# Kernel tuning notes

Hardware: AMD Instinct MI355X
Metric: run time of the kernel (lower is better)

Reference implementation:

```python
import jax, jax.numpy as jnp
import numpy as np

DIM = 1024   # dim
T = 16       # maximum_time_steps
NT = 64      # num_templates
B = 2048     # batch
S = 77       # words per sentence


def setup_inputs() -> dict:
    key = jax.random.key(0)
    ks = jax.random.split(key, 16)
    p = lambda k, shp: jax.random.normal(k, shp, dtype=jnp.float32) * 0.02
    return {
        "text_feats": jax.random.normal(ks[0], (B, S, DIM), dtype=jnp.float32),
        "text_sentence_feats": jax.random.normal(ks[1], (B, DIM), dtype=jnp.float32),
        "textual_query": jax.random.normal(ks[2], (B, DIM), dtype=jnp.float32),
        "time_step": jax.random.randint(ks[3], (B,), 0, T),
        "W1_w": p(ks[4], (T, DIM, DIM)),   # T stacked [out,in] linears
        "W1_b": p(ks[5], (T, DIM)),
        "W2_w": p(ks[6], (DIM, 2 * DIM)),
        "W2_b": p(ks[7], (DIM,)),
        "m1_w": p(ks[8], (DIM, DIM)),
        "m1_b": p(ks[9], (DIM,)),
        "m2_w": p(ks[10], (DIM, DIM)),
        "m2_b": p(ks[11], (DIM,)),
        "m3_w": p(ks[12], (NT, DIM)),
        "m3_b": p(ks[13], (NT,)),
        "attn_w": p(ks[14], (1, DIM)),
        "attn_b": p(ks[15], (1,)),
    }


def reference(text_feats, text_sentence_feats, textual_query, time_step,
              W1_w, W1_b, W2_w, W2_b, m1_w, m1_b, m2_w, m2_b, m3_w, m3_b,
              attn_w, attn_b):
    # Time-indexed linear: T is small, so compute all T projections for every
    # sample and select per-sample (avoids materializing a [B,DIM,DIM] gather).
    all_proj = jnp.einsum('bc,toc->tbo', text_sentence_feats, W1_w) + W1_b[:, None, :]  # t b d
    x1 = jnp.take_along_axis(all_proj, time_step[None, :, None], axis=0)[0]  # b d
    # concat with textual query, project back to dim
    x = jnp.concatenate([x1, textual_query], axis=-1) @ W2_w.T + W2_b  # b d
    # 3-layer MLP -> template distribution
    h = jax.nn.relu(x @ m1_w.T + m1_b)
    h = jax.nn.relu(h @ m2_w.T + m2_b)
    template_distribution = jax.nn.softmax(h @ m3_w.T + m3_b, axis=-1)  # b #templates
    # soft attention over words: score each (x * word_feat) with a linear
    x_w = x[:, None, :] * text_feats  # b s c
    scores = jnp.einsum('bsc,c->bs', x_w, attn_w[0]) + attn_b[0]
    words_soft_distribution = jax.nn.softmax(scores, axis=-1)  # b s
    c_t = jnp.einsum('bs,bsc->bc', words_soft_distribution, text_feats)  # b c
    return template_distribution, words_soft_distribution, c_t
```

## Files before the change

kernel.cpp:

```cpp
#include <hip/hip_runtime.h>
#include <stdint.h>

typedef __bf16 bf16;
typedef bf16 bf16x8 __attribute__((ext_vector_type(8)));
typedef bf16 bf16x4 __attribute__((ext_vector_type(4)));
typedef float f32x4 __attribute__((ext_vector_type(4)));

#define DIM   1024
#define TMAX  16
#define NTPL  64
#define BATCH 2048
#define SLEN  77

__device__ __forceinline__ void gl_lds16(const void* g, void* l) {
  __builtin_amdgcn_global_load_lds(
      (const __attribute__((address_space(1))) void*)g,
      (__attribute__((address_space(3))) void*)l, 16, 0, 0);
}

__global__ void bucket_k(const int* __restrict__ ts, int* __restrict__ perm,
                         int* __restrict__ bstart) {
  __shared__ int cnt[TMAX], base[TMAX], cur[TMAX];
  int tid = threadIdx.x;
  if (tid < TMAX) { cnt[tid] = 0; cur[tid] = 0; }
  __syncthreads();
  for (int b = tid; b < BATCH; b += 256) atomicAdd(&cnt[ts[b]], 1);
  __syncthreads();
  if (tid == 0) {
    int a = 0;
    for (int t = 0; t < TMAX; ++t) { base[t] = a; bstart[t] = a; a += cnt[t]; }
    bstart[TMAX] = a;
  }
  __syncthreads();
  for (int b = tid; b < BATCH; b += 256) {
    int t = ts[b];
    perm[base[t] + atomicAdd(&cur[t], 1)] = b;
  }
}

__global__ void cvt_bf16_k(const float* __restrict__ src, bf16* __restrict__ dst) {
  int idx = blockIdx.x * 256 + threadIdx.x;
  float4 v = ((const float4*)src)[idx];
  bf16x4 o = {(bf16)v.x, (bf16)v.y, (bf16)v.z, (bf16)v.w};
  ((bf16x4*)dst)[idx] = o;
}

__global__ void cvt_tq_k(const float* __restrict__ tq, bf16* __restrict__ xcat) {
  int idx = blockIdx.x * 256 + threadIdx.x;
  int b = idx >> 8, c4 = idx & 255;
  float4 v = ((const float4*)(tq + (size_t)b * DIM))[c4];
  bf16x4 o = {(bf16)v.x, (bf16)v.y, (bf16)v.z, (bf16)v.w};
  *(bf16x4*)(xcat + (size_t)b * 2 * DIM + DIM + c4 * 4) = o;
}

__global__ __launch_bounds__(256, 2) void gemm_bt(
    const bf16* __restrict__ A, int lda, const bf16* __restrict__ B, int ldb,
    const float* __restrict__ bias, bf16* __restrict__ C, int ldc,
    float* __restrict__ Cf, int N, int K, int relu) {
  __shared__ bf16 As[128 * 32];
  __shared__ bf16 Bs[128 * 32];
  const int tid = threadIdx.x;
  const int rowBase = blockIdx.y * 128, colBase = blockIdx.x * 128;

  const bf16* ag[2]; const bf16* bg[2];
  bf16* al[2]; bf16* bl[2];
#pragma unroll
  for (int i = 0; i < 2; ++i) {
    int j = tid + i * 256;
    int r = j >> 2, kq = j & 3;
    ag[i] = A + (size_t)(rowBase + r) * lda + kq * 8;
    int bn = colBase + r; if (bn > N - 1) bn = N - 1;
    bg[i] = B + (size_t)bn * ldb + kq * 8;
    al[i] = As + j * 8;
    bl[i] = Bs + j * 8;
  }
  const int wave = tid >> 6, lane = tid & 63;
  const int wm = wave >> 1, wn = wave & 1;
  const int mr = lane & 15, quad = lane >> 4;

  f32x4 acc[4][4];
#pragma unroll
  for (int i = 0; i < 4; ++i)
#pragma unroll
    for (int j = 0; j < 4; ++j) acc[i][j] = (f32x4){0.f, 0.f, 0.f, 0.f};

  for (int k0 = 0; k0 < K; k0 += 32) {
    __syncthreads();
#pragma unroll
    for (int i = 0; i < 2; ++i) {
      gl_lds16(ag[i] + k0, al[i]);
      gl_lds16(bg[i] + k0, bl[i]);
    }
    __syncthreads();
    bf16x8 af[4], bfr[4];
#pragma unroll
    for (int i = 0; i < 4; ++i)
      af[i] = *(const bf16x8*)&As[(wm * 64 + i * 16 + mr) * 32 + quad * 8];
#pragma unroll
    for (int j = 0; j < 4; ++j)
      bfr[j] = *(const bf16x8*)&Bs[(wn * 64 + j * 16 + mr) * 32 + quad * 8];
#pragma unroll
    for (int i = 0; i < 4; ++i)
#pragma unroll
      for (int j = 0; j < 4; ++j)
        acc[i][j] = __builtin_amdgcn_mfma_f32_16x16x32_bf16(af[i], bfr[j], acc[i][j], 0, 0, 0);
  }

  const int r0 = quad * 4;
#pragma unroll
  for (int i = 0; i < 4; ++i) {
    int gm = rowBase + wm * 64 + i * 16 + r0;
#pragma unroll
    for (int j = 0; j < 4; ++j) {
      int gn = colBase + wn * 64 + j * 16 + mr;
      if (gn < N) {
        float bv = bias ? bias[gn] : 0.f;
#pragma unroll
        for (int r = 0; r < 4; ++r) {
          float v = acc[i][j][r] + bv;
          if (relu) v = fmaxf(v, 0.f);
          C[(size_t)(gm + r) * ldc + gn] = (bf16)v;
          if (Cf) Cf[(size_t)(gm + r) * ldc + gn] = v;
        }
      }
    }
  }
}

__global__ __launch_bounds__(256, 2) void gemm_stage1(
    const bf16* __restrict__ tsbf, const bf16* __restrict__ W1bf,
    const float* __restrict__ W1b, const int* __restrict__ perm,
    const int* __restrict__ bstart, bf16* __restrict__ xcat) {
  const int t = blockIdx.z;
  const int s0 = bstart[t];
  const int cnt = bstart[t + 1] - s0;
  const int by = blockIdx.y;
  if (by * 128 >= cnt) return;
  __shared__ bf16 As[128 * 32];
  __shared__ bf16 Bs[128 * 32];
  const int tid = threadIdx.x;
  const int colBase = blockIdx.x * 128;
  const bf16* Bmat = W1bf + ((size_t)t << 20);

  const bf16* ag[2]; const bf16* bg[2];
  bf16* al[2]; bf16* bl[2];
#pragma unroll
  for (int i = 0; i < 2; ++i) {
    int j = tid + i * 256;
    int r = j >> 2, kq = j & 3;
    int lr = by * 128 + r;
    int src = perm[s0 + (lr < cnt ? lr : 0)];
    ag[i] = tsbf + (size_t)src * DIM + kq * 8;
    bg[i] = Bmat + (size_t)(colBase + r) * DIM + kq * 8;
    al[i] = As + j * 8;
    bl[i] = Bs + j * 8;
  }
  const int wave = tid >> 6, lane = tid & 63;
  const int wm = wave >> 1, wn = wave & 1;
  const int mr = lane & 15, quad = lane >> 4;

  f32x4 acc[4][4];
#pragma unroll
  for (int i = 0; i < 4; ++i)
#pragma unroll
    for (int j = 0; j < 4; ++j) acc[i][j] = (f32x4){0.f, 0.f, 0.f, 0.f};

  for (int k0 = 0; k0 < DIM; k0 += 32) {
    __syncthreads();
#pragma unroll
    for (int i = 0; i < 2; ++i) {
      gl_lds16(ag[i] + k0, al[i]);
      gl_lds16(bg[i] + k0, bl[i]);
    }
    __syncthreads();
    bf16x8 af[4], bfr[4];
#pragma unroll
    for (int i = 0; i < 4; ++i)
      af[i] = *(const bf16x8*)&As[(wm * 64 + i * 16 + mr) * 32 + quad * 8];
#pragma unroll
    for (int j = 0; j < 4; ++j)
      bfr[j] = *(const bf16x8*)&Bs[(wn * 64 + j * 16 + mr) * 32 + quad * 8];
#pragma unroll
    for (int i = 0; i < 4; ++i)
#pragma unroll
      for (int j = 0; j < 4; ++j)
        acc[i][j] = __builtin_amdgcn_mfma_f32_16x16x32_bf16(af[i], bfr[j], acc[i][j], 0, 0, 0);
  }

  const int r0 = quad * 4;
#pragma unroll
  for (int i = 0; i < 4; ++i) {
    int lr = by * 128 + wm * 64 + i * 16 + r0;
#pragma unroll
    for (int j = 0; j < 4; ++j) {
      int gn = colBase + wn * 64 + j * 16 + mr;
      float bv = W1b[t * DIM + gn];
#pragma unroll
      for (int r = 0; r < 4; ++r) {
        if (lr + r < cnt) {
          int bidx = perm[s0 + lr + r];
          xcat[(size_t)bidx * 2 * DIM + gn] = (bf16)(acc[i][j][r] + bv);
        }
      }
    }
  }
}

__global__ __launch_bounds__(256) void softmax64_k(const bf16* __restrict__ logits,
                                                   float* __restrict__ out) {
  int row = blockIdx.x * 4 + (threadIdx.x >> 6);
  int lane = threadIdx.x & 63;
  float v = (float)logits[row * NTPL + lane];
  float mx = v;
#pragma unroll
  for (int o = 32; o; o >>= 1) mx = fmaxf(mx, __shfl_xor(mx, o));
  float e = __expf(v - mx);
  float s = e;
#pragma unroll
  for (int o = 32; o; o >>= 1) s += __shfl_xor(s, o);
  out[row * NTPL + lane] = e / s;
}

__global__ __launch_bounds__(256) void attn_k(
    const float* __restrict__ x, const float* __restrict__ attn_w,
    const float* __restrict__ attn_b, const float* __restrict__ feats,
    float* __restrict__ words, float* __restrict__ ct) {
  const int b = blockIdx.x;
  const int tid = threadIdx.x;
  const float* fb = feats + (size_t)b * SLEN * DIM;
  float4 aw = ((const float4*)attn_w)[tid];
  float4 xv = ((const float4*)(x + (size_t)b * DIM))[tid];
  const float v0 = xv.x * aw.x, v1 = xv.y * aw.y, v2 = xv.z * aw.z, v3 = xv.w * aw.w;
  const float ab = attn_b[0];
  __shared__ float red[4];
  __shared__ float sc[SLEN];
  const int wave = tid >> 6, lane = tid & 63;
  float m = -1e30f, l = 0.f;
  float a0 = 0.f, a1 = 0.f, a2 = 0.f, a3 = 0.f;
  float4 f = ((const float4*)fb)[tid];
  for (int s = 0; s < SLEN; ++s) {
    float4 fn = make_float4(0.f, 0.f, 0.f, 0.f);
    if (s + 1 < SLEN) fn = ((const float4*)(fb + (size_t)(s + 1) * DIM))[tid];
    float p = f.x * v0 + f.y * v1 + f.z * v2 + f.w * v3;
#pragma unroll
    for (int o = 32; o; o >>= 1) p += __shfl_down(p, o);
    if (lane == 0) red[wave] = p;
    __syncthreads();
    float score = red[0] + red[1] + red[2] + red[3] + ab;
    __syncthreads();
    if (tid == 0) sc[s] = score;
    float mn = fmaxf(m, score);
    float scale = __expf(m - mn);
    float w = __expf(score - mn);
    l = l * scale + w;
    a0 = a0 * scale + w * f.x;
    a1 = a1 * scale + w * f.y;
    a2 = a2 * scale + w * f.z;
    a3 = a3 * scale + w * f.w;
    m = mn;
    f = fn;
  }
  __syncthreads();
  float inv = 1.f / l;
  if (tid < SLEN) words[(size_t)b * SLEN + tid] = __expf(sc[tid] - m) * inv;
  float4 o; o.x = a0 * inv; o.y = a1 * inv; o.z = a2 * inv; o.w = a3 * inv;
  ((float4*)(ct + (size_t)b * DIM))[tid] = o;
}

extern "C" void kernel_launch(void* const* d_in, const int* in_sizes, int n_in,
                              void* d_out, int out_size, void* d_ws, size_t ws_size,
                              hipStream_t stream) {
  const float* feats = (const float*)d_in[0];
  const float* tsent = (const float*)d_in[1];
  const float* tq    = (const float*)d_in[2];
  const int*   tstep = (const int*)d_in[3];
  const float* W1w = (const float*)d_in[4];
  const float* W1b = (const float*)d_in[5];
  const float* W2w = (const float*)d_in[6];
  const float* W2b = (const float*)d_in[7];
  const float* m1w = (const float*)d_in[8];
  const float* m1b = (const float*)d_in[9];
  const float* m2w = (const float*)d_in[10];
  const float* m2b = (const float*)d_in[11];
  const float* m3w = (const float*)d_in[12];
  const float* m3b = (const float*)d_in[13];
  const float* attw = (const float*)d_in[14];
  const float* attb = (const float*)d_in[15];

  char* p = (char*)d_ws;
  auto alloc = [&](size_t bytes) { char* q = p; p += (bytes + 255) & ~(size_t)255; return q; };
  int*  perm   = (int*)alloc(BATCH * 4);
  int*  bstart = (int*)alloc(17 * 4);
  bf16* tsbf = (bf16*)alloc((size_t)BATCH * DIM * 2);
  bf16* W1bf = (bf16*)alloc((size_t)TMAX * DIM * DIM * 2);
  bf16* W2bf = (bf16*)alloc((size_t)DIM * 2 * DIM * 2);
  bf16* m1bf = (bf16*)alloc((size_t)DIM * DIM * 2);
  bf16* m2bf = (bf16*)alloc((size_t)DIM * DIM * 2);
  bf16* m3bf = (bf16*)alloc((size_t)NTPL * DIM * 2);
  bf16* xcat = (bf16*)alloc((size_t)BATCH * 2 * DIM * 2);
  bf16* xbf  = (bf16*)alloc((size_t)BATCH * DIM * 2);
  float* xf  = (float*)alloc((size_t)BATCH * DIM * 4);
  bf16* h1   = (bf16*)alloc((size_t)BATCH * DIM * 2);
  bf16* h2   = (bf16*)alloc((size_t)BATCH * DIM * 2);
  bf16* lg   = (bf16*)alloc((size_t)BATCH * NTPL * 2);

  float* out_td = (float*)d_out;
  float* out_w  = out_td + (size_t)BATCH * NTPL;
  float* out_ct = out_w + (size_t)BATCH * SLEN;

  bucket_k<<<1, 256, 0, stream>>>(tstep, perm, bstart);
  cvt_bf16_k<<<(TMAX * DIM * DIM) / 1024, 256, 0, stream>>>(W1w, W1bf);
  cvt_bf16_k<<<(BATCH * DIM) / 1024, 256, 0, stream>>>(tsent, tsbf);
  cvt_bf16_k<<<(DIM * 2 * DIM) / 1024, 256, 0, stream>>>(W2w, W2bf);
  cvt_bf16_k<<<(DIM * DIM) / 1024, 256, 0, stream>>>(m1w, m1bf);
  cvt_bf16_k<<<(DIM * DIM) / 1024, 256, 0, stream>>>(m2w, m2bf);
  cvt_bf16_k<<<(NTPL * DIM) / 1024, 256, 0, stream>>>(m3w, m3bf);
  cvt_tq_k<<<(BATCH * DIM) / 1024, 256, 0, stream>>>(tq, xcat);

  gemm_stage1<<<dim3(DIM / 128, BATCH / 128, TMAX), 256, 0, stream>>>(
      tsbf, W1bf, W1b, perm, bstart, xcat);
  gemm_bt<<<dim3(DIM / 128, BATCH / 128), 256, 0, stream>>>(
      xcat, 2 * DIM, W2bf, 2 * DIM, W2b, xbf, DIM, xf, DIM, 2 * DIM, 0);
  gemm_bt<<<dim3(DIM / 128, BATCH / 128), 256, 0, stream>>>(
      xbf, DIM, m1bf, DIM, m1b, h1, DIM, nullptr, DIM, DIM, 1);
  gemm_bt<<<dim3(DIM / 128, BATCH / 128), 256, 0, stream>>>(
      h1, DIM, m2bf, DIM, m2b, h2, DIM, nullptr, DIM, DIM, 1);
  gemm_bt<<<dim3(1, BATCH / 128), 256, 0, stream>>>(
      h2, DIM, m3bf, DIM, m3b, lg, NTPL, nullptr, NTPL, DIM, 0);
  softmax64_k<<<BATCH / 4, 256, 0, stream>>>(lg, out_td);
  attn_k<<<BATCH, 256, 0, stream>>>(xf, attw, attb, feats, out_w, out_ct);
}
```

Measured before the change: 1.073 ms.

## Fuse fp32-to-bf16 conversion into GEMM loads, fuse softmax, parallelize attention

```diff
diff --git a/kernel.cpp b/kernel.cpp
--- a/kernel.cpp
+++ b/kernel.cpp
@@ -16,6 +16,12 @@
   __builtin_amdgcn_global_load_lds(
       (const __attribute__((address_space(1))) void*)g,
       (__attribute__((address_space(3))) void*)l, 16, 0, 0);
+}
+
+__device__ __forceinline__ bf16x8 cvt8(float4 u, float4 w) {
+  bf16x8 o = {(bf16)u.x, (bf16)u.y, (bf16)u.z, (bf16)u.w,
+              (bf16)w.x, (bf16)w.y, (bf16)w.z, (bf16)w.w};
+  return o;
 }
 
 __global__ void bucket_k(const int* __restrict__ ts, int* __restrict__ perm,
@@ -38,13 +44,6 @@
   }
 }
 
-__global__ void cvt_bf16_k(const float* __restrict__ src, bf16* __restrict__ dst) {
-  int idx = blockIdx.x * 256 + threadIdx.x;
-  float4 v = ((const float4*)src)[idx];
-  bf16x4 o = {(bf16)v.x, (bf16)v.y, (bf16)v.z, (bf16)v.w};
-  ((bf16x4*)dst)[idx] = o;
-}
-
 __global__ void cvt_tq_k(const float* __restrict__ tq, bf16* __restrict__ xcat) {
   int idx = blockIdx.x * 256 + threadIdx.x;
   int b = idx >> 8, c4 = idx & 255;
@@ -53,82 +52,8 @@
   *(bf16x4*)(xcat + (size_t)b * 2 * DIM + DIM + c4 * 4) = o;
 }
 
-__global__ __launch_bounds__(256, 2) void gemm_bt(
-    const bf16* __restrict__ A, int lda, const bf16* __restrict__ B, int ldb,
-    const float* __restrict__ bias, bf16* __restrict__ C, int ldc,
-    float* __restrict__ Cf, int N, int K, int relu) {
-  __shared__ bf16 As[128 * 32];
-  __shared__ bf16 Bs[128 * 32];
-  const int tid = threadIdx.x;
-  const int rowBase = blockIdx.y * 128, colBase = blockIdx.x * 128;
-
-  const bf16* ag[2]; const bf16* bg[2];
-  bf16* al[2]; bf16* bl[2];
-#pragma unroll
-  for (int i = 0; i < 2; ++i) {
-    int j = tid + i * 256;
-    int r = j >> 2, kq = j & 3;
-    ag[i] = A + (size_t)(rowBase + r) * lda + kq * 8;
-    int bn = colBase + r; if (bn > N - 1) bn = N - 1;
-    bg[i] = B + (size_t)bn * ldb + kq * 8;
-    al[i] = As + j * 8;
-    bl[i] = Bs + j * 8;
-  }
-  const int wave = tid >> 6, lane = tid & 63;
-  const int wm = wave >> 1, wn = wave & 1;
-  const int mr = lane & 15, quad = lane >> 4;
-
-  f32x4 acc[4][4];
-#pragma unroll
-  for (int i = 0; i < 4; ++i)
-#pragma unroll
-    for (int j = 0; j < 4; ++j) acc[i][j] = (f32x4){0.f, 0.f, 0.f, 0.f};
-
-  for (int k0 = 0; k0 < K; k0 += 32) {
-    __syncthreads();
-#pragma unroll
-    for (int i = 0; i < 2; ++i) {
-      gl_lds16(ag[i] + k0, al[i]);
-      gl_lds16(bg[i] + k0, bl[i]);
-    }
-    __syncthreads();
-    bf16x8 af[4], bfr[4];
-#pragma unroll
-    for (int i = 0; i < 4; ++i)
-      af[i] = *(const bf16x8*)&As[(wm * 64 + i * 16 + mr) * 32 + quad * 8];
-#pragma unroll
-    for (int j = 0; j < 4; ++j)
-      bfr[j] = *(const bf16x8*)&Bs[(wn * 64 + j * 16 + mr) * 32 + quad * 8];
-#pragma unroll
-    for (int i = 0; i < 4; ++i)
-#pragma unroll
-      for (int j = 0; j < 4; ++j)
-        acc[i][j] = __builtin_amdgcn_mfma_f32_16x16x32_bf16(af[i], bfr[j], acc[i][j], 0, 0, 0);
-  }
-
-  const int r0 = quad * 4;
-#pragma unroll
-  for (int i = 0; i < 4; ++i) {
-    int gm = rowBase + wm * 64 + i * 16 + r0;
-#pragma unroll
-    for (int j = 0; j < 4; ++j) {
-      int gn = colBase + wn * 64 + j * 16 + mr;
-      if (gn < N) {
-        float bv = bias ? bias[gn] : 0.f;
-#pragma unroll
-        for (int r = 0; r < 4; ++r) {
-          float v = acc[i][j][r] + bv;
-          if (relu) v = fmaxf(v, 0.f);
-          C[(size_t)(gm + r) * ldc + gn] = (bf16)v;
-          if (Cf) Cf[(size_t)(gm + r) * ldc + gn] = v;
-        }
-      }
-    }
-  }
-}
-
-__global__ __launch_bounds__(256, 2) void gemm_stage1(
-    const bf16* __restrict__ tsbf, const bf16* __restrict__ W1bf,
+__global__ __launch_bounds__(256, 2) void gemm_s1(
+    const float* __restrict__ tsent, const float* __restrict__ W1w,
     const float* __restrict__ W1b, const int* __restrict__ perm,
     const int* __restrict__ bstart, bf16* __restrict__ xcat) {
   const int t = blockIdx.z;
@@ -140,9 +65,9 @@
   __shared__ bf16 Bs[128 * 32];
   const int tid = threadIdx.x;
   const int colBase = blockIdx.x * 128;
-  const bf16* Bmat = W1bf + ((size_t)t << 20);
-
-  const bf16* ag[2]; const bf16* bg[2];
+  const float* Bmat = W1w + (size_t)t * DIM * DIM;
+
+  const float* agf[2]; const float* bgf[2];
   bf16* al[2]; bf16* bl[2];
 #pragma unroll
   for (int i = 0; i < 2; ++i) {
@@ -150,8 +75,8 @@
     int r = j >> 2, kq = j & 3;
     int lr = by * 128 + r;
     int src = perm[s0 + (lr < cnt ? lr : 0)];
-    ag[i] = tsbf + (size_t)src * DIM + kq * 8;
-    bg[i] = Bmat + (size_t)(colBase + r) * DIM + kq * 8;
+    agf[i] = tsent + (size_t)src * DIM + kq * 8;
+    bgf[i] = Bmat + (size_t)(colBase + r) * DIM + kq * 8;
     al[i] = As + j * 8;
     bl[i] = Bs + j * 8;
   }
@@ -169,8 +94,12 @@
     __syncthreads();
 #pragma unroll
     for (int i = 0; i < 2; ++i) {
-      gl_lds16(ag[i] + k0, al[i]);
-      gl_lds16(bg[i] + k0, bl[i]);
+      float4 ua = *(const float4*)(agf[i] + k0);
+      float4 wa = *(const float4*)(agf[i] + k0 + 4);
+      float4 ub = *(const float4*)(bgf[i] + k0);
+      float4 wb = *(const float4*)(bgf[i] + k0 + 4);
+      *(bf16x8*)al[i] = cvt8(ua, wa);
+      *(bf16x8*)bl[i] = cvt8(ub, wb);
     }
     __syncthreads();
     bf16x8 af[4], bfr[4];
@@ -206,19 +135,153 @@
   }
 }
 
-__global__ __launch_bounds__(256) void softmax64_k(const bf16* __restrict__ logits,
-                                                   float* __restrict__ out) {
-  int row = blockIdx.x * 4 + (threadIdx.x >> 6);
-  int lane = threadIdx.x & 63;
-  float v = (float)logits[row * NTPL + lane];
-  float mx = v;
-#pragma unroll
-  for (int o = 32; o; o >>= 1) mx = fmaxf(mx, __shfl_xor(mx, o));
-  float e = __expf(v - mx);
-  float s = e;
-#pragma unroll
-  for (int o = 32; o; o >>= 1) s += __shfl_xor(s, o);
-  out[row * NTPL + lane] = e / s;
+__global__ __launch_bounds__(256, 2) void gemm_bt_bf(
+    const bf16* __restrict__ A, int lda, const float* __restrict__ Bf, int ldb,
+    const float* __restrict__ bias, bf16* __restrict__ C, int ldc,
+    float* __restrict__ Cf, int K, int relu) {
+  __shared__ bf16 As[128 * 32];
+  __shared__ bf16 Bs[128 * 32];
+  const int tid = threadIdx.x;
+  const int rowBase = blockIdx.y * 128, colBase = blockIdx.x * 128;
+
+  const bf16* ag[2]; const float* bgf[2];
+  bf16* al[2]; bf16* bl[2];
+#pragma unroll
+  for (int i = 0; i < 2; ++i) {
+    int j = tid + i * 256;
+    int r = j >> 2, kq = j & 3;
+    ag[i] = A + (size_t)(rowBase + r) * lda + kq * 8;
+    bgf[i] = Bf + (size_t)(colBase + r) * ldb + kq * 8;
+    al[i] = As + j * 8;
+    bl[i] = Bs + j * 8;
+  }
+  const int wave = tid >> 6, lane = tid & 63;
+  const int wm = wave >> 1, wn = wave & 1;
+  const int mr = lane & 15, quad = lane >> 4;
+
+  f32x4 acc[4][4];
+#pragma unroll
+  for (int i = 0; i < 4; ++i)
+#pragma unroll
+    for (int j = 0; j < 4; ++j) acc[i][j] = (f32x4){0.f, 0.f, 0.f, 0.f};
+
+  for (int k0 = 0; k0 < K; k0 += 32) {
+    __syncthreads();
+#pragma unroll
+    for (int i = 0; i < 2; ++i) {
+      gl_lds16(ag[i] + k0, al[i]);
+      float4 ub = *(const float4*)(bgf[i] + k0);
+      float4 wb = *(const float4*)(bgf[i] + k0 + 4);
+      *(bf16x8*)bl[i] = cvt8(ub, wb);
+    }
+    __syncthreads();
+    bf16x8 af[4], bfr[4];
+#pragma unroll
+    for (int i = 0; i < 4; ++i)
+      af[i] = *(const bf16x8*)&As[(wm * 64 + i * 16 + mr) * 32 + quad * 8];
+#pragma unroll
+    for (int j = 0; j < 4; ++j)
+      bfr[j] = *(const bf16x8*)&Bs[(wn * 64 + j * 16 + mr) * 32 + quad * 8];
+#pragma unroll
+    for (int i = 0; i < 4; ++i)
+#pragma unroll
+      for (int j = 0; j < 4; ++j)
+        acc[i][j] = __builtin_amdgcn_mfma_f32_16x16x32_bf16(af[i], bfr[j], acc[i][j], 0, 0, 0);
+  }
+
+  const int r0 = quad * 4;
+#pragma unroll
+  for (int i = 0; i < 4; ++i) {
+    int gm = rowBase + wm * 64 + i * 16 + r0;
+#pragma unroll
+    for (int j = 0; j < 4; ++j) {
+      int gn = colBase + wn * 64 + j * 16 + mr;
+      float bv = bias[gn];
+#pragma unroll
+      for (int r = 0; r < 4; ++r) {
+        float v = acc[i][j][r] + bv;
+        if (relu) v = fmaxf(v, 0.f);
+        C[(size_t)(gm + r) * ldc + gn] = (bf16)v;
+        if (Cf) Cf[(size_t)(gm + r) * ldc + gn] = v;
+      }
+    }
+  }
+}
+
+__global__ __launch_bounds__(256, 2) void gemm_m3_sm(
+    const bf16* __restrict__ A, const float* __restrict__ Bf,
+    const float* __restrict__ bias, float* __restrict__ out) {
+  __shared__ bf16 As[128 * 32];
+  __shared__ bf16 Bs[64 * 32];
+  __shared__ float lg[128][NTPL + 1];
+  const int tid = threadIdx.x;
+  const int rowBase = blockIdx.x * 128;
+
+  const bf16* ag[2]; bf16* al[2];
+#pragma unroll
+  for (int i = 0; i < 2; ++i) {
+    int j = tid + i * 256;
+    int r = j >> 2, kq = j & 3;
+    ag[i] = A + (size_t)(rowBase + r) * DIM + kq * 8;
+    al[i] = As + j * 8;
+  }
+  const float* bgf = Bf + (size_t)(tid >> 2) * DIM + (tid & 3) * 8;
+  bf16* bl = Bs + tid * 8;
+
+  const int wave = tid >> 6, lane = tid & 63;
+  const int mr = lane & 15, quad = lane >> 4;
+
+  f32x4 acc[2][4];
+#pragma unroll
+  for (int i = 0; i < 2; ++i)
+#pragma unroll
+    for (int j = 0; j < 4; ++j) acc[i][j] = (f32x4){0.f, 0.f, 0.f, 0.f};
+
+  for (int k0 = 0; k0 < DIM; k0 += 32) {
+    __syncthreads();
+    gl_lds16(ag[0] + k0, al[0]);
+    gl_lds16(ag[1] + k0, al[1]);
+    {
+      float4 ub = *(const float4*)(bgf + k0);
+      float4 wb = *(const float4*)(bgf + k0 + 4);
+      *(bf16x8*)bl = cvt8(ub, wb);
+    }
+    __syncthreads();
+    bf16x8 af[2], bfr[4];
+#pragma unroll
+    for (int i = 0; i < 2; ++i)
+      af[i] = *(const bf16x8*)&As[(wave * 32 + i * 16 + mr) * 32 + quad * 8];
+#pragma unroll
+    for (int j = 0; j < 4; ++j)
+      bfr[j] = *(const bf16x8*)&Bs[(j * 16 + mr) * 32 + quad * 8];
+#pragma unroll
+    for (int i = 0; i < 2; ++i)
+#pragma unroll
+      for (int j = 0; j < 4; ++j)
+        acc[i][j] = __builtin_amdgcn_mfma_f32_16x16x32_bf16(af[i], bfr[j], acc[i][j], 0, 0, 0);
+  }
+
+#pragma unroll
+  for (int i = 0; i < 2; ++i)
+#pragma unroll
+    for (int j = 0; j < 4; ++j) {
+      float bv = bias[j * 16 + mr];
+#pragma unroll
+      for (int r = 0; r < 4; ++r)
+        lg[wave * 32 + i * 16 + quad * 4 + r][j * 16 + mr] = acc[i][j][r] + bv;
+    }
+  __syncthreads();
+  for (int row = wave; row < 128; row += 4) {
+    float v = lg[row][lane];
+    float mx = v;
+#pragma unroll
+    for (int o = 32; o; o >>= 1) mx = fmaxf(mx, __shfl_xor(mx, o));
+    float e = __expf(v - mx);
+    float s = e;
+#pragma unroll
+    for (int o = 32; o; o >>= 1) s += __shfl_xor(s, o);
+    out[(size_t)(rowBase + row) * NTPL + lane] = e / s;
+  }
 }
 
 __global__ __launch_bounds__(256) void attn_k(
@@ -227,44 +290,75 @@
     float* __restrict__ words, float* __restrict__ ct) {
   const int b = blockIdx.x;
   const int tid = threadIdx.x;
+  const int wave = tid >> 6, lane = tid & 63;
   const float* fb = feats + (size_t)b * SLEN * DIM;
-  float4 aw = ((const float4*)attn_w)[tid];
-  float4 xv = ((const float4*)(x + (size_t)b * DIM))[tid];
-  const float v0 = xv.x * aw.x, v1 = xv.y * aw.y, v2 = xv.z * aw.z, v3 = xv.w * aw.w;
+
+  float4 v[4], acc[4];
+#pragma unroll
+  for (int q = 0; q < 4; ++q) {
+    float4 xv = *(const float4*)(x + (size_t)b * DIM + q * 256 + lane * 4);
+    float4 aw = *(const float4*)(attn_w + q * 256 + lane * 4);
+    v[q].x = xv.x * aw.x; v[q].y = xv.y * aw.y;
+    v[q].z = xv.z * aw.z; v[q].w = xv.w * aw.w;
+    acc[q] = make_float4(0.f, 0.f, 0.f, 0.f);
+  }
   const float ab = attn_b[0];
-  __shared__ float red[4];
+
   __shared__ float sc[SLEN];
-  const int wave = tid >> 6, lane = tid & 63;
+  __shared__ float sm[4], sl[4];
+  __shared__ float sacc[4][DIM];
+
   float m = -1e30f, l = 0.f;
-  float a0 = 0.f, a1 = 0.f, a2 = 0.f, a3 = 0.f;
-  float4 f = ((const float4*)fb)[tid];
-  for (int s = 0; s < SLEN; ++s) {
-    float4 fn = make_float4(0.f, 0.f, 0.f, 0.f);
-    if (s + 1 < SLEN) fn = ((const float4*)(fb + (size_t)(s + 1) * DIM))[tid];
-    float p = f.x * v0 + f.y * v1 + f.z * v2 + f.w * v3;
-#pragma unroll
-    for (int o = 32; o; o >>= 1) p += __shfl_down(p, o);
-    if (lane == 0) red[wave] = p;
-    __syncthreads();
-    float score = red[0] + red[1] + red[2] + red[3] + ab;
-    __syncthreads();
-    if (tid == 0) sc[s] = score;
+  for (int s = wave; s < SLEN; s += 4) {
+    const float* fr = fb + (size_t)s * DIM;
+    float4 f[4];
+    float p = 0.f;
+#pragma unroll
+    for (int q = 0; q < 4; ++q) {
+      f[q] = *(const float4*)(fr + q * 256 + lane * 4);
+      p += f[q].x * v[q].x + f[q].y * v[q].y + f[q].z * v[q].z + f[q].w * v[q].w;
+    }
+#pragma unroll
+    for (int o = 32; o; o >>= 1) p += __shfl_xor(p, o);
+    float score = p + ab;
+    if (lane == 0) sc[s] = score;
     float mn = fmaxf(m, score);
     float scale = __expf(m - mn);
     float w = __expf(score - mn);
     l = l * scale + w;
-    a0 = a0 * scale + w * f.x;
-    a1 = a1 * scale + w * f.y;
-    a2 = a2 * scale + w * f.z;
-    a3 = a3 * scale + w * f.w;
+#pragma unroll
+    for (int q = 0; q < 4; ++q) {
+      acc[q].x = acc[q].x * scale + w * f[q].x;
+      acc[q].y = acc[q].y * scale + w * f[q].y;
+      acc[q].z = acc[q].z * scale + w * f[q].z;
+      acc[q].w = acc[q].w * scale + w * f[q].w;
+    }
     m = mn;
-    f = fn;
-  }
+  }
+  if (lane == 0) { sm[wave] = m; sl[wave] = l; }
+#pragma unroll
+  for (int q = 0; q < 4; ++q)
+    *(float4*)&sacc[wave][q * 256 + lane * 4] = acc[q];
   __syncthreads();
-  float inv = 1.f / l;
-  if (tid < SLEN) words[(size_t)b * SLEN + tid] = __expf(sc[tid] - m) * inv;
-  float4 o; o.x = a0 * inv; o.y = a1 * inv; o.z = a2 * inv; o.w = a3 * inv;
-  ((float4*)(ct + (size_t)b * DIM))[tid] = o;
+
+  float M = fmaxf(fmaxf(sm[0], sm[1]), fmaxf(sm[2], sm[3]));
+  float e0 = __expf(sm[0] - M), e1 = __expf(sm[1] - M);
+  float e2 = __expf(sm[2] - M), e3 = __expf(sm[3] - M);
+  float L = sl[0] * e0 + sl[1] * e1 + sl[2] * e2 + sl[3] * e3;
+  float invL = 1.f / L;
+
+  if (tid < SLEN) words[(size_t)b * SLEN + tid] = __expf(sc[tid] - M) * invL;
+
+  float4 a0 = *(float4*)&sacc[0][tid * 4];
+  float4 a1 = *(float4*)&sacc[1][tid * 4];
+  float4 a2 = *(float4*)&sacc[2][tid * 4];
+  float4 a3 = *(float4*)&sacc[3][tid * 4];
+  float4 o;
+  o.x = (a0.x * e0 + a1.x * e1 + a2.x * e2 + a3.x * e3) * invL;
+  o.y = (a0.y * e0 + a1.y * e1 + a2.y * e2 + a3.y * e3) * invL;
+  o.z = (a0.z * e0 + a1.z * e1 + a2.z * e2 + a3.z * e3) * invL;
+  o.w = (a0.w * e0 + a1.w * e1 + a2.w * e2 + a3.w * e3) * invL;
+  *(float4*)(ct + (size_t)b * DIM + tid * 4) = o;
 }
 
 extern "C" void kernel_launch(void* const* d_in, const int* in_sizes, int n_in,
@@ -291,42 +385,26 @@
   auto alloc = [&](size_t bytes) { char* q = p; p += (bytes + 255) & ~(size_t)255; return q; };
   int*  perm   = (int*)alloc(BATCH * 4);
   int*  bstart = (int*)alloc(17 * 4);
-  bf16* tsbf = (bf16*)alloc((size_t)BATCH * DIM * 2);
-  bf16* W1bf = (bf16*)alloc((size_t)TMAX * DIM * DIM * 2);
-  bf16* W2bf = (bf16*)alloc((size_t)DIM * 2 * DIM * 2);
-  bf16* m1bf = (bf16*)alloc((size_t)DIM * DIM * 2);
-  bf16* m2bf = (bf16*)alloc((size_t)DIM * DIM * 2);
-  bf16* m3bf = (bf16*)alloc((size_t)NTPL * DIM * 2);
   bf16* xcat = (bf16*)alloc((size_t)BATCH * 2 * DIM * 2);
   bf16* xbf  = (bf16*)alloc((size_t)BATCH * DIM * 2);
   float* xf  = (float*)alloc((size_t)BATCH * DIM * 4);
   bf16* h1   = (bf16*)alloc((size_t)BATCH * DIM * 2);
   bf16* h2   = (bf16*)alloc((size_t)BATCH * DIM * 2);
-  bf16* lg   = (bf16*)alloc((size_t)BATCH * NTPL * 2);
 
   float* out_td = (float*)d_out;
   float* out_w  = out_td + (size_t)BATCH * NTPL;
   float* out_ct = out_w + (size_t)BATCH * SLEN;
 
   bucket_k<<<1, 256, 0, stream>>>(tstep, perm, bstart);
-  cvt_bf16_k<<<(TMAX * DIM * DIM) / 1024, 256, 0, stream>>>(W1w, W1bf);
-  cvt_bf16_k<<<(BATCH * DIM) / 1024, 256, 0, stream>>>(tsent, tsbf);
-  cvt_bf16_k<<<(DIM * 2 * DIM) / 1024, 256, 0, stream>>>(W2w, W2bf);
-  cvt_bf16_k<<<(DIM * DIM) / 1024, 256, 0, stream>>>(m1w, m1bf);
-  cvt_bf16_k<<<(DIM * DIM) / 1024, 256, 0, stream>>>(m2w, m2bf);
-  cvt_bf16_k<<<(NTPL * DIM) / 1024, 256, 0, stream>>>(m3w, m3bf);
   cvt_tq_k<<<(BATCH * DIM) / 1024, 256, 0, stream>>>(tq, xcat);
-
-  gemm_stage1<<<dim3(DIM / 128, BATCH / 128, TMAX), 256, 0, stream>>>(
-      tsbf, W1bf, W1b, perm, bstart, xcat);
-  gemm_bt<<<dim3(DIM / 128, BATCH / 128), 256, 0, stream>>>(
-      xcat, 2 * DIM, W2bf, 2 * DIM, W2b, xbf, DIM, xf, DIM, 2 * DIM, 0);
-  gemm_bt<<<dim3(DIM / 128, BATCH / 128), 256, 0, stream>>>(
-      xbf, DIM, m1bf, DIM, m1b, h1, DIM, nullptr, DIM, DIM, 1);
-  gemm_bt<<<dim3(DIM / 128, BATCH / 128), 256, 0, stream>>>(
-      h1, DIM, m2bf, DIM, m2b, h2, DIM, nullptr, DIM, DIM, 1);
-  gemm_bt<<<dim3(1, BATCH / 128), 256, 0, stream>>>(
-      h2, DIM, m3bf, DIM, m3b, lg, NTPL, nullptr, NTPL, DIM, 0);
-  softmax64_k<<<BATCH / 4, 256, 0, stream>>>(lg, out_td);
+  gemm_s1<<<dim3(DIM / 128, BATCH / 128, TMAX), 256, 0, stream>>>(
+      tsent, W1w, W1b, perm, bstart, xcat);
+  gemm_bt_bf<<<dim3(DIM / 128, BATCH / 128), 256, 0, stream>>>(
+      xcat, 2 * DIM, W2w, 2 * DIM, W2b, xbf, DIM, xf, 2 * DIM, 0);
   attn_k<<<BATCH, 256, 0, stream>>>(xf, attw, attb, feats, out_w, out_ct);
-}
+  gemm_bt_bf<<<dim3(DIM / 128, BATCH / 128), 256, 0, stream>>>(
+      xbf, DIM, m1w, DIM, m1b, h1, DIM, nullptr, DIM, 1);
+  gemm_bt_bf<<<dim3(DIM / 128, BATCH / 128), 256, 0, stream>>>(
+      h1, DIM, m2w, DIM, m2b, h2, DIM, nullptr, DIM, 1);
+  gemm_m3_sm<<<BATCH / 128, 256, 0, stream>>>(h2, m3w, m3b, out_td);
+}
```

Measured after the change: 1.188 ms. +10.7%, slower.
